# Kernel tuning notes

Hardware: AMD Instinct MI355X
Metric: run time of the kernel (lower is better)

The kernel has to match this reference:

```python
import math
import jax, jax.numpy as jnp
import numpy as np

N = 1600; C_IN = 16; HID = 64; OUT = 64; D_K = 8; N_HEADS = 8
CUTS = 8; NUM_RBF = 8; RBF_PROJ = 4; RADIUS = 6.0; ALPHA = 3.0

def leaky(x):
    return jnp.where(x >= 0, x, 0.2 * x)

def group_norm(x, gamma, beta, groups=4, eps=1e-5):
    # x: [N, C]; torch GroupNorm applied on [1, C, N]: stats over (C/groups, N) per group
    n, c = x.shape
    xg = x.T.reshape(groups, -1)
    mu = jnp.mean(xg, axis=1, keepdims=True)
    var = jnp.mean((xg - mu) ** 2, axis=1, keepdims=True)
    xn = ((xg - mu) * jax.lax.rsqrt(var + eps)).reshape(c, n).T
    return xn * gamma + beta

def setup_inputs():
    key = jax.random.key(0)
    ks = jax.random.split(key, 32)
    def rn(k, shape, s=0.1):
        return (jax.random.normal(k, shape) * s).astype(jnp.float32)
    return {
        "points": jax.random.normal(ks[0], (N, 3), jnp.float32),
        "nuv": jax.random.normal(ks[1], (N, 3, 3), jnp.float32),
        "features": jax.random.normal(ks[2], (N, C_IN), jnp.float32),
        "w_in1": rn(ks[3], (HID, C_IN)), "b_in1": rn(ks[4], (HID,)),
        "w_in2": rn(ks[5], (HID, HID)), "b_in2": rn(ks[6], (HID,)),
        "g_in": 1.0 + rn(ks[7], (HID,)), "be_in": rn(ks[8], (HID,)),
        "wq": rn(ks[9], (HID, HID)), "bq": rn(ks[10], (HID,)),
        "wk": rn(ks[11], (HID, HID)), "bk": rn(ks[12], (HID,)),
        "wv": rn(ks[13], (HID, HID)), "bv": rn(ks[14], (HID,)),
        "conv_w1": rn(ks[15], (CUTS, 4 + RBF_PROJ), 0.5),
        "conv_b1": jnp.abs(rn(ks[16], (CUTS,), 0.5)),
        "conv_w2": rn(ks[17], (HID, CUTS), 0.3), "conv_b2": rn(ks[18], (HID,), 0.3),
        "rbf_log_sigma": jnp.log(jnp.asarray(0.6 * 2.0 / (NUM_RBF - 1), jnp.float32)),
        "rbf_a": rn(ks[19], (RBF_PROJ, NUM_RBF), 0.3), "rbf_b": rn(ks[20], (RBF_PROJ,), 0.1),
        "rbf_centers": jnp.linspace(0.0, 2.0, NUM_RBF, dtype=jnp.float32),
        "w_o1": rn(ks[21], (OUT, HID)), "b_o1": rn(ks[22], (OUT,)),
        "w_o2": rn(ks[23], (OUT, OUT)), "b_o2": rn(ks[24], (OUT,)),
        "g_out": 1.0 + rn(ks[25], (OUT,)), "be_out": rn(ks[26], (OUT,)),
        "w_res": rn(ks[27], (OUT, C_IN)), "b_res": rn(ks[28], (OUT,)),
    }

def reference(points, nuv, features, w_in1, b_in1, w_in2, b_in2, g_in, be_in,
              wq, bq, wk, bk, wv, bv, conv_w1, conv_b1, conv_w2, conv_b2,
              rbf_log_sigma, rbf_a, rbf_b, rbf_centers,
              w_o1, b_o1, w_o2, b_o2, g_out, be_out, w_res, b_res):
    # point-wise MLP + GroupNorm
    h = leaky(features @ w_in1.T + b_in1)
    h = leaky(h @ w_in2.T + b_in2)
    h = group_norm(h, g_in, be_in)
    Q = h @ wq.T + bq
    K = h @ wk.T + bk
    V = h @ wv.T + bv
    pts = points / (math.sqrt(2.0) * RADIUS)
    diff = pts[None, :, :] - pts[:, None, :]            # [N, N, 3] = x_j - x_i
    n_i = nuv[:, 0, :]
    n_j = jax.lax.stop_gradient(n_i)                    # j-side normals are detached in the original
    ndot = jnp.einsum("ia,ja->ij", n_i, n_j)            # <n_i, n_j>
    d2 = jnp.sum(diff ** 2, axis=-1) * (2.0 - ndot) ** 2  # pseudo-geodesic squared distance
    W = (1.0 + d2 / ALPHA) ** (-ALPHA)                  # geodesic window weight
    d2_safe = jnp.where(d2 > 0, d2, 1.0)
    base_d = jnp.where(d2 > 0, jnp.sqrt(d2_safe), 0.0)  # safe sqrt (finite grad at 0)
    sigma = jnp.maximum(jnp.exp(rbf_log_sigma), 1e-6)
    R = jnp.exp(-((base_d[:, :, None] - rbf_centers) ** 2) / (2.0 * sigma ** 2))  # [N,N,NUM_RBF]
    R_proj = R @ rbf_a.T + rbf_b                        # [N, N, RBF_PROJ]
    X_loc = jnp.einsum("iab,ijb->ija", nuv, diff)       # local tangent-frame coords [N,N,3]
    X = jnp.concatenate([X_loc, ndot[:, :, None], R_proj], axis=-1)  # [N, N, 4+RBF_PROJ]
    F1 = jax.nn.relu(X @ conv_w1.T + conv_b1)           # shared conv layer-1 [N, N, CUTS]
    scale = 1.0 / math.sqrt(D_K)
    heads = []
    for h_id in range(N_HEADS):
        s = slice(h_id * D_K, (h_id + 1) * D_K)
        Fh = jax.nn.relu(F1 @ conv_w2[s].T + conv_b2[s])      # per-head conv weights [N, N, D_K]
        S = (Q[:, s] @ K[:, s].T) * scale                     # attention logits [N, N]
        P = jax.nn.softmax(S, axis=1) * W                     # softmax over j, fused with window
        heads.append(jnp.einsum("ij,ijc,jc->ic", P, Fh, V[:, s]))
    agg = jnp.concatenate(heads, axis=1)                      # [N, HID]
    o = leaky(agg @ w_o1.T + b_o1)
    o = leaky(o @ w_o2.T + b_o2)
    o = group_norm(o, g_out, be_out)
    return o + features @ w_res.T + b_res
```

## Files before the change

### kernel.cpp

```cpp
#include <hip/hip_runtime.h>

typedef __fp16 h2 __attribute__((ext_vector_type(2)));
typedef unsigned int u32;
typedef unsigned short u16;

#define NPTS 1600
#define NCHUNK 10
#define CHUNKJ 160
#define TILE 32
#define QS (0.35355339059327373f*1.4426950408889634f)
#define PSCALE 0.11785113019775793f
#define LOG2E 1.4426950408889634f

__device__ __forceinline__ float leaky(float x){ return x >= 0.f ? x : 0.2f*x; }
__device__ __forceinline__ float d4(float4 a, float4 b){ return a.x*b.x + a.y*b.y + a.z*b.z + a.w*b.w; }
__device__ __forceinline__ u32 pkn(float a, float b){ h2 v; v[0]=(__fp16)a; v[1]=(__fp16)b; return __builtin_bit_cast(u32,v); }
__device__ __forceinline__ h2 u2h(u32 u){ return __builtin_bit_cast(h2,u); }
__device__ __forceinline__ float dot2(h2 a, h2 b, float c){ return __builtin_amdgcn_fdot2(a,b,c,false); }
__device__ __forceinline__ u32 rfl(u32 x){ return (u32)__builtin_amdgcn_readfirstlane((int)x); }

__global__ __launch_bounds__(256) void k_in(
    const float* __restrict__ feat, const float* __restrict__ w1, const float* __restrict__ b1,
    const float* __restrict__ w2, const float* __restrict__ b2,
    const float* __restrict__ conv_w1, const float* __restrict__ conv_b1,
    const float* __restrict__ conv_w2,
    const float* __restrict__ rbf_a, const float* __restrict__ rbf_b,
    const float* __restrict__ rbf_ls, const float* __restrict__ rbf_c,
    float* __restrict__ h2out, float* __restrict__ bstat1, float* __restrict__ wpk)
{
  __shared__ float sh[4][64];
  __shared__ float sred[4][8];
  int t = threadIdx.x, w = t>>6, c = t&63;
  int i = blockIdx.x*4 + w;

  if (blockIdx.x == 0) {
    u32* wp = (u32*)wpk;
    {
      int row = t>>2, q = t&3;
      wp[32 + row*4 + q] = pkn(conv_w2[row*8+2*q], conv_w2[row*8+2*q+1]);
    }
    if (t < 32) {
      int cc = t>>2, kq = t&3;
      float a0=0.f, a1=0.f;
      #pragma unroll
      for (int p=0;p<4;p++){ a0 += conv_w1[cc*8+4+p]*rbf_a[p*8+2*kq]; a1 += conv_w1[cc*8+4+p]*rbf_a[p*8+2*kq+1]; }
      wp[cc*4+kq] = pkn(a0,a1);
    } else if (t < 40) {
      int cc = t-32; float s = conv_b1[cc];
      #pragma unroll
      for (int p=0;p<4;p++) s += conv_w1[cc*8+4+p]*rbf_b[p];
      wpk[288+cc] = s;
    } else if (t == 40) {
      float sig = fmaxf(expf(rbf_ls[0]), 1e-6f);
      float m = -LOG2E/(2.f*sig*sig);
      float c0 = rbf_c[0];
      float dl = rbf_c[1] - rbf_c[0];
      float A1v = m*dl*dl;
      wpk[296] = c0;
      wpk[297] = m;
      wpk[298] = -2.f*m*dl;
      wpk[299] = A1v;
      float Av = exp2f(A1v);
      wpk[300] = Av;
      wpk[301] = Av*Av;
    }
  }

  const float4* f4 = (const float4*)(feat + i*16);
  float4 f0=f4[0], f1v=f4[1], f2v=f4[2], f3v=f4[3];
  const float4* w1r = (const float4*)(w1 + c*16);
  float h1 = b1[c] + d4(f0,w1r[0]) + d4(f1v,w1r[1]) + d4(f2v,w1r[2]) + d4(f3v,w1r[3]);
  h1 = leaky(h1);
  sh[w][c] = h1;
  __syncthreads();
  float hh = b2[c];
  #pragma unroll
  for (int k4=0;k4<16;k4++){
    float4 hv = *(const float4*)&sh[w][k4*4];
    hh += d4(hv, *(const float4*)&w2[c*64 + k4*4]);
  }
  hh = leaky(hh);
  h2out[i*64+c] = hh;

  float s = hh, qq = hh*hh;
  s += __shfl_xor(s,1);  qq += __shfl_xor(qq,1);
  s += __shfl_xor(s,2);  qq += __shfl_xor(qq,2);
  s += __shfl_xor(s,4);  qq += __shfl_xor(qq,4);
  s += __shfl_xor(s,8);  qq += __shfl_xor(qq,8);
  if ((c&15)==0){ int g=c>>4; sred[w][g]=s; sred[w][4+g]=qq; }
  __syncthreads();
  if (t<8) bstat1[blockIdx.x*8+t] = sred[0][t]+sred[1][t]+sred[2][t]+sred[3][t];
}

__global__ __launch_bounds__(256) void k_qkv(
  const float* __restrict__ h2b, const float* __restrict__ bstat1,
  const float* __restrict__ g_in, const float* __restrict__ be_in,
  const float* __restrict__ wq, const float* __restrict__ bq,
  const float* __restrict__ wk, const float* __restrict__ bk,
  const float* __restrict__ wv, const float* __restrict__ bv,
  const float* __restrict__ pts, const float* __restrict__ nuv,
  u32* __restrict__ Q16, u32* __restrict__ K16, u32* __restrict__ V16,
  float* __restrict__ PN)
{
  __shared__ float sh[4][64];
  __shared__ float sp[64];
  __shared__ float sst[8];
  int t=threadIdx.x, w=t>>6, c=t&63;
  int i = blockIdx.x*4 + w;
  if (t<64){ int g=t&7; float s=0.f;
    for (int m=t>>3; m<400; m+=8) s += bstat1[m*8+g];
    sp[t]=s; }
  __syncthreads();
  if (t<8){ float s=0.f;
    #pragma unroll
    for (int q=0;q<8;q++) s += sp[q*8+t];
    sst[t]=s; }
  __syncthreads();
  int g = c>>4;
  const float inv = 1.f/25600.f;
  float mu = sst[g]*inv;
  float var = sst[4+g]*inv - mu*mu;
  float rs = rsqrtf(var + 1e-5f);
  float hn = (h2b[i*64+c]-mu)*rs*g_in[c] + be_in[c];
  sh[w][c] = hn;
  __syncthreads();
  float q=bq[c], k=bk[c], v=bv[c];
  #pragma unroll
  for (int k4=0;k4<16;k4++){
    float4 hv = *(const float4*)&sh[w][k4*4];
    q += d4(hv, *(const float4*)&wq[c*64+k4*4]);
    k += d4(hv, *(const float4*)&wk[c*64+k4*4]);
    v += d4(hv, *(const float4*)&wv[c*64+k4*4]);
  }
  u16* Q16u = (u16*)Q16;
  u16* K16u = (u16*)K16;
  u16* V16u = (u16*)V16;
  __fp16 qh = (__fp16)(q*QS);
  __fp16 kh = (__fp16)k;
  __fp16 vh = (__fp16)v;
  Q16u[i*64 + c] = __builtin_bit_cast(u16, qh);
  K16u[i*64 + c] = __builtin_bit_cast(u16, kh);
  int pr = ((i>>5)<<4) + (i&15);
  int hf = (i>>4)&1;
  V16u[(pr*64 + c)*2 + hf] = __builtin_bit_cast(u16, vh);
  if (c < 6){
    float pv = (c<3) ? pts[i*3+c]*PSCALE : nuv[i*9+(c-3)];
    PN[i*8+c] = pv;
  } else if (c < 8) PN[i*8+c] = 0.f;
}

__global__ __launch_bounds__(256) void k_pair(
  const u32* __restrict__ Q16, const u32* __restrict__ K16, const u32* __restrict__ V16,
  const float* __restrict__ PN, const float* __restrict__ nuv,
  const float* __restrict__ w1, const float* __restrict__ wpk,
  const float* __restrict__ b2g, float* __restrict__ part)
{
  __shared__ __align__(16) u32   sQ16[16*36];
  __shared__ __align__(16) u32   sWX[16*20];
  __shared__ __align__(16) float sRedH[4*16*36];

  int t = threadIdx.x;
  int r = t & 15, jl = t >> 4;
  int bx = blockIdx.x;
  int rb = bx % 100, jc = bx / 100;
  int I0 = rb*16, J0 = jc*CHUNKJ;
  int i = I0 + r;

  if (t < 128) {
    int qrow = t>>3, qq4 = (t&7)<<2;
    *(uint4*)&sQ16[qrow*36+qq4] = *(const uint4*)&Q16[(I0+qrow)*32+qq4];
  }
  if (t < 128) {
    int r2 = t>>3, cc = t&7, ib = (I0+r2)*9;
    float a0=w1[cc*8], a1=w1[cc*8+1], a2=w1[cc*8+2];
    float x = a0*nuv[ib+0] + a1*nuv[ib+3] + a2*nuv[ib+6];
    float y = a0*nuv[ib+1] + a1*nuv[ib+4] + a2*nuv[ib+7];
    float z = a0*nuv[ib+2] + a1*nuv[ib+5] + a2*nuv[ib+8];
    sWX[r2*20+cc*2+0] = pkn(x,y);
    sWX[r2*20+cc*2+1] = pkn(z, w1[cc*8+3]);
  }
  __syncthreads();

  const u32* wp = (const u32*)wpk;
  h2 wr[8][4];
  #pragma unroll
  for (int cc=0;cc<8;cc++)
    #pragma unroll
    for (int q2=0;q2<4;q2++) wr[cc][q2] = u2h(rfl(wp[cc*4+q2]));
  const u32* w2p = wp + 32;
  const float* b1p = wpk + 288;
  float c0  = wpk[296];
  float mco = wpk[297];
  float C2  = wpk[298];
  float Af  = wpk[300];
  float A2f = wpk[301];

  float4 pni0 = *(const float4*)&PN[i*8];
  float4 pni1 = *(const float4*)&PN[i*8+4];
  float pix = pni0.x, piy = pni0.y, piz = pni0.z;
  float nix = pni0.w, niy = pni1.x, niz = pni1.y;

  #pragma unroll 1
  for (int hp=0; hp<2; hp++) {
    float acc[32];
    #pragma unroll
    for (int o=0;o<32;o++) acc[o] = 0.f;
    float lh[4] = {0.f,0.f,0.f,0.f};

    #pragma unroll 1
    for (int tb=0; tb<CHUNKJ; tb+=TILE) {
      int jbase = J0 + tb;
      int jA = jbase + jl;
      int jB = jA + 16;

      h2 F1p[2][4];
      float Wv[2];
      #pragma unroll
      for (int jj=0;jj<2;jj++) {
        int j = jj ? jB : jA;
        float4 a0 = *(const float4*)&PN[j*8];
        float4 a1 = *(const float4*)&PN[j*8+4];
        float dx = a0.x-pix, dy = a0.y-piy, dz = a0.z-piz;
        float ndot = nix*a0.w + niy*a1.x + niz*a1.y;
        float d2r = dx*dx + dy*dy + dz*dz;
        float wf = 2.f - ndot;
        float d2 = d2r*wf*wf;
        float tp = fmaf(d2, 0.3333333333333333f, 1.f);
        Wv[jj] = __builtin_amdgcn_rcpf(tp*tp*tp);
        float dd = __builtin_amdgcn_sqrtf(d2);
        float g0 = dd - c0;
        float E = __builtin_amdgcn_exp2f(mco*g0*g0);
        float U = __builtin_amdgcn_exp2f(C2*g0);
        float R[8];
        R[0] = E;
        float tt = U*Af;
        #pragma unroll
        for (int k=1;k<8;k++){ R[k] = R[k-1]*tt; tt *= A2f; }
        h2 xv0; xv0[0]=(__fp16)dx; xv0[1]=(__fp16)dy;
        h2 xv1; xv1[0]=(__fp16)dz; xv1[1]=(__fp16)ndot;
        h2 r01=__builtin_amdgcn_cvt_pkrtz(R[0],R[1]);
        h2 r23=__builtin_amdgcn_cvt_pkrtz(R[2],R[3]);
        h2 r45=__builtin_amdgcn_cvt_pkrtz(R[4],R[5]);
        h2 r67=__builtin_amdgcn_cvt_pkrtz(R[6],R[7]);
        float F1f[8];
        #pragma unroll
        for (int cc=0;cc<8;cc++){
          uint2 wx2 = *(const uint2*)&sWX[r*20+cc*2];
          float fa = dot2(r01, wr[cc][0], dot2(r23, wr[cc][1], b1p[cc]));
          float fb = dot2(r45, wr[cc][2], dot2(r67, wr[cc][3], 0.f));
          float fc = dot2(u2h(wx2.x), xv0, dot2(u2h(wx2.y), xv1, 0.f));
          F1f[cc] = fmaxf(fa+fb+fc, 0.f);
        }
        F1p[jj][0]=__builtin_amdgcn_cvt_pkrtz(F1f[0],F1f[1]);
        F1p[jj][1]=__builtin_amdgcn_cvt_pkrtz(F1f[2],F1f[3]);
        F1p[jj][2]=__builtin_amdgcn_cvt_pkrtz(F1f[4],F1f[5]);
        F1p[jj][3]=__builtin_amdgcn_cvt_pkrtz(F1f[6],F1f[7]);
      }
      h2 Wvp = __builtin_amdgcn_cvt_pkrtz(Wv[0], Wv[1]);

      const u32* kArow = &K16[jA*32];
      const u32* kBrow = &K16[jB*32];
      const u32* vrow  = &V16[(((u32)jbase>>1)+jl)*64];

      #pragma unroll
      for (int hh=0; hh<4; hh++) {
        int h = (hp<<2) + hh;
        uint4 qh = *(const uint4*)&sQ16[r*36 + (h<<2)];
        uint4 kA = *(const uint4*)&kArow[h<<2];
        uint4 kB = *(const uint4*)&kBrow[h<<2];
        float S0 = dot2(u2h(qh.x),u2h(kA.x), dot2(u2h(qh.y),u2h(kA.y), 0.f))
                 + dot2(u2h(qh.z),u2h(kA.z), dot2(u2h(qh.w),u2h(kA.w), 0.f));
        float S1 = dot2(u2h(qh.x),u2h(kB.x), dot2(u2h(qh.y),u2h(kB.y), 0.f))
                 + dot2(u2h(qh.z),u2h(kB.z), dot2(u2h(qh.w),u2h(kB.w), 0.f));
        float e0 = __builtin_amdgcn_exp2f(S0);
        float e1 = __builtin_amdgcn_exp2f(S1);
        lh[hh] += e0 + e1;
        h2 ewp = __builtin_amdgcn_cvt_pkrtz(e0,e1) * Wvp;
        uint4 vpA = *(const uint4*)&vrow[h*8];
        uint4 vpB = *(const uint4*)&vrow[h*8+4];
        u32 vparr[8] = {vpA.x,vpA.y,vpA.z,vpA.w,vpB.x,vpB.y,vpB.z,vpB.w};
        #pragma unroll
        for (int cc=0;cc<8;cc++){
          int rw = h*8+cc;
          h2 w0=u2h(w2p[rw*4+0]), w1h=u2h(w2p[rw*4+1]), w2h=u2h(w2p[rw*4+2]), w3h=u2h(w2p[rw*4+3]);
          float b2v = b2g[rw];
          float fh0 = dot2(F1p[0][0],w0, dot2(F1p[0][1],w1h, b2v))
                    + dot2(F1p[0][2],w2h, dot2(F1p[0][3],w3h, 0.f));
          float fh1 = dot2(F1p[1][0],w0, dot2(F1p[1][1],w1h, b2v))
                    + dot2(F1p[1][2],w2h, dot2(F1p[1][3],w3h, 0.f));
          h2 fhp = __builtin_amdgcn_cvt_pkrtz(fmaxf(fh0,0.f), fmaxf(fh1,0.f));
          h2 ev = u2h(vparr[cc]) * ewp;
          acc[hh*8+cc] = dot2(fhp, ev, acc[hh*8+cc]);
        }
      }
    }

    #pragma unroll
    for (int o=0;o<32;o++){ acc[o] += __shfl_xor(acc[o],16); acc[o] += __shfl_xor(acc[o],32); }
    #pragma unroll
    for (int hh=0;hh<4;hh++){ lh[hh] += __shfl_xor(lh[hh],16); lh[hh] += __shfl_xor(lh[hh],32); }
    __syncthreads();
    int wv = t >> 6, lane = t & 63;
    if (lane < 16) {
      #pragma unroll
      for (int o=0;o<32;o++) sRedH[(wv*16+lane)*36+o] = acc[o];
      #pragma unroll
      for (int hh=0;hh<4;hh++) sRedH[(wv*16+lane)*36+32+hh] = lh[hh];
    }
    __syncthreads();
    for (int v2 = t; v2 < 16*36; v2 += 256) {
      int rr = v2/36, o = v2 - rr*36;
      float s = sRedH[(0*16+rr)*36+o]+sRedH[(1*16+rr)*36+o]+sRedH[(2*16+rr)*36+o]+sRedH[(3*16+rr)*36+o];
      int off = (o < 32) ? (hp<<5)+o : 64 + (hp<<2) + (o-32);
      part[(jc*NPTS + I0 + rr)*72 + off] = s;
    }
  }
}

__global__ __launch_bounds__(256) void k_agg(
  const float* __restrict__ part, const float* __restrict__ w_o1, const float* __restrict__ b_o1,
  const float* __restrict__ w_o2, const float* __restrict__ b_o2,
  float* __restrict__ o2b, float* __restrict__ bstat2)
{
  __shared__ float sh[4][64];
  __shared__ float sred[4][8];
  int t = threadIdx.x, w = t>>6, c = t&63;
  int i = blockIdx.x*4 + w;
  int h = c>>3;
  float a = 0.f, L = 0.f;
  #pragma unroll
  for (int jc=0;jc<NCHUNK;jc++){
    const float* p = part + (jc*NPTS + i)*72;
    a += p[c]; L += p[64+h];
  }
  float agg = a / L;
  sh[w][c] = agg; __syncthreads();
  float o1 = b_o1[c];
  #pragma unroll
  for (int k4=0;k4<16;k4++){
    float4 hv = *(const float4*)&sh[w][k4*4];
    o1 += d4(hv, *(const float4*)&w_o1[c*64+k4*4]);
  }
  o1 = leaky(o1);
  __syncthreads();
  sh[w][c] = o1; __syncthreads();
  float o2 = b_o2[c];
  #pragma unroll
  for (int k4=0;k4<16;k4++){
    float4 hv = *(const float4*)&sh[w][k4*4];
    o2 += d4(hv, *(const float4*)&w_o2[c*64+k4*4]);
  }
  o2 = leaky(o2);
  o2b[i*64+c] = o2;

  float s = o2, qq = o2*o2;
  s += __shfl_xor(s,1);  qq += __shfl_xor(qq,1);
  s += __shfl_xor(s,2);  qq += __shfl_xor(qq,2);
  s += __shfl_xor(s,4);  qq += __shfl_xor(qq,4);
  s += __shfl_xor(s,8);  qq += __shfl_xor(qq,8);
  if ((c&15)==0){ int g=c>>4; sred[w][g]=s; sred[w][4+g]=qq; }
  __syncthreads();
  if (t<8) bstat2[blockIdx.x*8+t] = sred[0][t]+sred[1][t]+sred[2][t]+sred[3][t];
}

__global__ __launch_bounds__(256) void k_out(
  const float* __restrict__ o2b, const float* __restrict__ bstat2,
  const float* __restrict__ g_out, const float* __restrict__ be_out,
  const float* __restrict__ feat, const float* __restrict__ w_res, const float* __restrict__ b_res,
  float* __restrict__ out)
{
  __shared__ float sp[64];
  __shared__ float sst[8];
  int t = threadIdx.x, w = t>>6, c = t&63;
  int i = blockIdx.x*4 + w;
  if (t<64){ int g=t&7; float s=0.f;
    for (int m=t>>3; m<400; m+=8) s += bstat2[m*8+g];
    sp[t]=s; }
  __syncthreads();
  if (t<8){ float s=0.f;
    #pragma unroll
    for (int q=0;q<8;q++) s += sp[q*8+t];
    sst[t]=s; }
  __syncthreads();
  int g = c>>4;
  const float inv = 1.f/25600.f;
  float mu = sst[g]*inv;
  float var = sst[4+g]*inv - mu*mu;
  float rs = rsqrtf(var + 1e-5f);
  float on = (o2b[i*64+c]-mu)*rs*g_out[c] + be_out[c];
  const float4* f4 = (const float4*)(feat + i*16);
  const float4* wr = (const float4*)(w_res + c*16);
  float res = b_res[c] + d4(f4[0],wr[0]) + d4(f4[1],wr[1]) + d4(f4[2],wr[2]) + d4(f4[3],wr[3]);
  out[i*64+c] = on + res;
}

extern "C" void kernel_launch(void* const* d_in, const int* in_sizes, int n_in,
                              void* d_out, int out_size, void* d_ws, size_t ws_size,
                              hipStream_t stream) {
  const float* points  = (const float*)d_in[0];
  const float* nuv     = (const float*)d_in[1];
  const float* feat    = (const float*)d_in[2];
  const float* w_in1   = (const float*)d_in[3];
  const float* b_in1   = (const float*)d_in[4];
  const float* w_in2   = (const float*)d_in[5];
  const float* b_in2   = (const float*)d_in[6];
  const float* g_in    = (const float*)d_in[7];
  const float* be_in   = (const float*)d_in[8];
  const float* wq      = (const float*)d_in[9];
  const float* bq      = (const float*)d_in[10];
  const float* wk      = (const float*)d_in[11];
  const float* bk      = (const float*)d_in[12];
  const float* wv      = (const float*)d_in[13];
  const float* bv      = (const float*)d_in[14];
  const float* conv_w1 = (const float*)d_in[15];
  const float* conv_b1 = (const float*)d_in[16];
  const float* conv_w2 = (const float*)d_in[17];
  const float* conv_b2 = (const float*)d_in[18];
  const float* rbf_ls  = (const float*)d_in[19];
  const float* rbf_a   = (const float*)d_in[20];
  const float* rbf_b   = (const float*)d_in[21];
  const float* rbf_c   = (const float*)d_in[22];
  const float* w_o1    = (const float*)d_in[23];
  const float* b_o1    = (const float*)d_in[24];
  const float* w_o2    = (const float*)d_in[25];
  const float* b_o2    = (const float*)d_in[26];
  const float* g_out   = (const float*)d_in[27];
  const float* be_out  = (const float*)d_in[28];
  const float* w_res   = (const float*)d_in[29];
  const float* b_res   = (const float*)d_in[30];

  float* ws     = (float*)d_ws;
  float* h2f    = ws;
  u32*   Q16    = (u32*)(ws + 102400);
  u32*   K16    = (u32*)(ws + 153600);
  u32*   V16    = (u32*)(ws + 204800);
  float* PN     = ws + 256000;
  float* bstat1 = ws + 268800;
  float* bstat2 = ws + 272000;
  float* wpk    = ws + 275200;
  float* part   = ws + 275520;
  float* o2b    = ws + 1427520;
  float* out    = (float*)d_out;

  k_in<<<400, 256, 0, stream>>>(feat, w_in1, b_in1, w_in2, b_in2,
                                conv_w1, conv_b1, conv_w2, rbf_a, rbf_b, rbf_ls, rbf_c,
                                h2f, bstat1, wpk);
  k_qkv<<<400, 256, 0, stream>>>(h2f, bstat1, g_in, be_in, wq, bq, wk, bk, wv, bv,
                                 points, nuv, Q16, K16, V16, PN);
  k_pair<<<1000, 256, 0, stream>>>(Q16, K16, V16, PN, nuv, conv_w1, wpk, conv_b2, part);
  k_agg<<<400, 256, 0, stream>>>(part, w_o1, b_o1, w_o2, b_o2, o2b, bstat2);
  k_out<<<400, 256, 0, stream>>>(o2b, bstat2, g_out, be_out, feat, w_res, b_res, out);
}
```

Baseline: 262.9 us.

## Fuse head-pair passes in pair kernel and widen blocks to 512 threads

The pair kernel used to make two passes over the j-chunk, four heads per pass, and so recomputed the geometric features (distances, RBF, conv layer 1) twice. It now keeps all 8 heads' 64 accumulators in registers and makes a single pass. Blocks grow to 512 threads with 320-wide j chunks, so half as many partial results are written and summed in k_agg, and the V layout is reshaped to match the 64-wide tile. The cost is a much larger register footprint per thread, which may lower occupancy or cause spills, and fewer blocks in the grid.

```diff
diff --git a/kernel.cpp b/kernel.cpp
--- a/kernel.cpp
+++ b/kernel.cpp
@@ -5,9 +5,9 @@
 typedef unsigned short u16;
 
 #define NPTS 1600
-#define NCHUNK 10
-#define CHUNKJ 160
-#define TILE 32
+#define NCHUNK 5
+#define CHUNKJ 320
+#define TILE 64
 #define QS (0.35355339059327373f*1.4426950408889634f)
 #define PSCALE 0.11785113019775793f
 #define LOG2E 1.4426950408889634f
@@ -140,8 +140,8 @@
   __fp16 vh = (__fp16)v;
   Q16u[i*64 + c] = __builtin_bit_cast(u16, qh);
   K16u[i*64 + c] = __builtin_bit_cast(u16, kh);
-  int pr = ((i>>5)<<4) + (i&15);
-  int hf = (i>>4)&1;
+  int pr = ((i>>6)<<5) + (i&31);
+  int hf = (i>>5)&1;
   V16u[(pr*64 + c)*2 + hf] = __builtin_bit_cast(u16, vh);
   if (c < 6){
     float pv = (c<3) ? pts[i*3+c]*PSCALE : nuv[i*9+(c-3)];
@@ -149,15 +149,16 @@
   } else if (c < 8) PN[i*8+c] = 0.f;
 }
 
-__global__ __launch_bounds__(256) void k_pair(
+__global__ __launch_bounds__(512) void k_pair(
   const u32* __restrict__ Q16, const u32* __restrict__ K16, const u32* __restrict__ V16,
   const float* __restrict__ PN, const float* __restrict__ nuv,
   const float* __restrict__ w1, const float* __restrict__ wpk,
   const float* __restrict__ b2g, float* __restrict__ part)
 {
-  __shared__ __align__(16) u32   sQ16[16*36];
-  __shared__ __align__(16) u32   sWX[16*20];
-  __shared__ __align__(16) float sRedH[4*16*36];
+  __shared__ __align__(16) float SM[8*16*72];
+  u32* sQ16 = (u32*)SM;
+  u32* sWX  = (u32*)SM + 576;
+  float* sRed = SM;
 
   int t = threadIdx.x;
   int r = t & 15, jl = t >> 4;
@@ -200,120 +201,119 @@
   float pix = pni0.x, piy = pni0.y, piz = pni0.z;
   float nix = pni0.w, niy = pni1.x, niz = pni1.y;
 
+  float acc[64];
+  #pragma unroll
+  for (int o=0;o<64;o++) acc[o] = 0.f;
+  float lh[8];
+  #pragma unroll
+  for (int h=0;h<8;h++) lh[h] = 0.f;
+
   #pragma unroll 1
-  for (int hp=0; hp<2; hp++) {
-    float acc[32];
-    #pragma unroll
-    for (int o=0;o<32;o++) acc[o] = 0.f;
-    float lh[4] = {0.f,0.f,0.f,0.f};
-
-    #pragma unroll 1
-    for (int tb=0; tb<CHUNKJ; tb+=TILE) {
-      int jbase = J0 + tb;
-      int jA = jbase + jl;
-      int jB = jA + 16;
-
-      h2 F1p[2][4];
-      float Wv[2];
+  for (int tb=0; tb<CHUNKJ; tb+=TILE) {
+    int jbase = J0 + tb;
+    int jA = jbase + jl;
+    int jB = jA + 32;
+
+    h2 F1p[2][4];
+    float Wv[2];
+    #pragma unroll
+    for (int jj=0;jj<2;jj++) {
+      int j = jj ? jB : jA;
+      float4 a0 = *(const float4*)&PN[j*8];
+      float4 a1 = *(const float4*)&PN[j*8+4];
+      float dx = a0.x-pix, dy = a0.y-piy, dz = a0.z-piz;
+      float ndot = nix*a0.w + niy*a1.x + niz*a1.y;
+      float d2r = dx*dx + dy*dy + dz*dz;
+      float wf = 2.f - ndot;
+      float d2 = d2r*wf*wf;
+      float tp = fmaf(d2, 0.3333333333333333f, 1.f);
+      Wv[jj] = __builtin_amdgcn_rcpf(tp*tp*tp);
+      float dd = __builtin_amdgcn_sqrtf(d2);
+      float g0 = dd - c0;
+      float E = __builtin_amdgcn_exp2f(mco*g0*g0);
+      float U = __builtin_amdgcn_exp2f(C2*g0);
+      float R[8];
+      R[0] = E;
+      float tt = U*Af;
       #pragma unroll
-      for (int jj=0;jj<2;jj++) {
-        int j = jj ? jB : jA;
-        float4 a0 = *(const float4*)&PN[j*8];
-        float4 a1 = *(const float4*)&PN[j*8+4];
-        float dx = a0.x-pix, dy = a0.y-piy, dz = a0.z-piz;
-        float ndot = nix*a0.w + niy*a1.x + niz*a1.y;
-        float d2r = dx*dx + dy*dy + dz*dz;
-        float wf = 2.f - ndot;
-        float d2 = d2r*wf*wf;
-        float tp = fmaf(d2, 0.3333333333333333f, 1.f);
-        Wv[jj] = __builtin_amdgcn_rcpf(tp*tp*tp);
-        float dd = __builtin_amdgcn_sqrtf(d2);
-        float g0 = dd - c0;
-        float E = __builtin_amdgcn_exp2f(mco*g0*g0);
-        float U = __builtin_amdgcn_exp2f(C2*g0);
-        float R[8];
-        R[0] = E;
-        float tt = U*Af;
-        #pragma unroll
-        for (int k=1;k<8;k++){ R[k] = R[k-1]*tt; tt *= A2f; }
-        h2 xv0; xv0[0]=(__fp16)dx; xv0[1]=(__fp16)dy;
-        h2 xv1; xv1[0]=(__fp16)dz; xv1[1]=(__fp16)ndot;
-        h2 r01=__builtin_amdgcn_cvt_pkrtz(R[0],R[1]);
-        h2 r23=__builtin_amdgcn_cvt_pkrtz(R[2],R[3]);
-        h2 r45=__builtin_amdgcn_cvt_pkrtz(R[4],R[5]);
-        h2 r67=__builtin_amdgcn_cvt_pkrtz(R[6],R[7]);
-        float F1f[8];
-        #pragma unroll
-        for (int cc=0;cc<8;cc++){
-          uint2 wx2 = *(const uint2*)&sWX[r*20+cc*2];
-          float fa = dot2(r01, wr[cc][0], dot2(r23, wr[cc][1], b1p[cc]));
-          float fb = dot2(r45, wr[cc][2], dot2(r67, wr[cc][3], 0.f));
-          float fc = dot2(u2h(wx2.x), xv0, dot2(u2h(wx2.y), xv1, 0.f));
-          F1f[cc] = fmaxf(fa+fb+fc, 0.f);
-        }
-        F1p[jj][0]=__builtin_amdgcn_cvt_pkrtz(F1f[0],F1f[1]);
-        F1p[jj][1]=__builtin_amdgcn_cvt_pkrtz(F1f[2],F1f[3]);
-        F1p[jj][2]=__builtin_amdgcn_cvt_pkrtz(F1f[4],F1f[5]);
-        F1p[jj][3]=__builtin_amdgcn_cvt_pkrtz(F1f[6],F1f[7]);
+      for (int k=1;k<8;k++){ R[k] = R[k-1]*tt; tt *= A2f; }
+      h2 xv0; xv0[0]=(__fp16)dx; xv0[1]=(__fp16)dy;
+      h2 xv1; xv1[0]=(__fp16)dz; xv1[1]=(__fp16)ndot;
+      h2 r01=__builtin_amdgcn_cvt_pkrtz(R[0],R[1]);
+      h2 r23=__builtin_amdgcn_cvt_pkrtz(R[2],R[3]);
+      h2 r45=__builtin_amdgcn_cvt_pkrtz(R[4],R[5]);
+      h2 r67=__builtin_amdgcn_cvt_pkrtz(R[6],R[7]);
+      float F1f[8];
+      #pragma unroll
+      for (int cc=0;cc<8;cc++){
+        uint2 wx2 = *(const uint2*)&sWX[r*20+cc*2];
+        float fa = dot2(r01, wr[cc][0], dot2(r23, wr[cc][1], b1p[cc]));
+        float fb = dot2(r45, wr[cc][2], dot2(r67, wr[cc][3], 0.f));
+        float fc = dot2(u2h(wx2.x), xv0, dot2(u2h(wx2.y), xv1, 0.f));
+        F1f[cc] = fmaxf(fa+fb+fc, 0.f);
       }
-      h2 Wvp = __builtin_amdgcn_cvt_pkrtz(Wv[0], Wv[1]);
-
-      const u32* kArow = &K16[jA*32];
-      const u32* kBrow = &K16[jB*32];
-      const u32* vrow  = &V16[(((u32)jbase>>1)+jl)*64];
-
+      F1p[jj][0]=__builtin_amdgcn_cvt_pkrtz(F1f[0],F1f[1]);
+      F1p[jj][1]=__builtin_amdgcn_cvt_pkrtz(F1f[2],F1f[3]);
+      F1p[jj][2]=__builtin_amdgcn_cvt_pkrtz(F1f[4],F1f[5]);
+      F1p[jj][3]=__builtin_amdgcn_cvt_pkrtz(F1f[6],F1f[7]);
+    }
+    h2 Wvp = __builtin_amdgcn_cvt_pkrtz(Wv[0], Wv[1]);
+
+    const u32* kArow = &K16[jA*32];
+    const u32* kBrow = &K16[jB*32];
+    const u32* vrow  = &V16[(((u32)jbase>>1)+jl)*64];
+
+    #pragma unroll
+    for (int h=0;h<8;h++) {
+      uint4 qh = *(const uint4*)&sQ16[r*36 + (h<<2)];
+      uint4 kA = *(const uint4*)&kArow[h<<2];
+      uint4 kB = *(const uint4*)&kBrow[h<<2];
+      float S0 = dot2(u2h(qh.x),u2h(kA.x), dot2(u2h(qh.y),u2h(kA.y), 0.f))
+               + dot2(u2h(qh.z),u2h(kA.z), dot2(u2h(qh.w),u2h(kA.w), 0.f));
+      float S1 = dot2(u2h(qh.x),u2h(kB.x), dot2(u2h(qh.y),u2h(kB.y), 0.f))
+               + dot2(u2h(qh.z),u2h(kB.z), dot2(u2h(qh.w),u2h(kB.w), 0.f));
+      float e0 = __builtin_amdgcn_exp2f(S0);
+      float e1 = __builtin_amdgcn_exp2f(S1);
+      lh[h] += e0 + e1;
+      h2 ewp = __builtin_amdgcn_cvt_pkrtz(e0,e1) * Wvp;
+      uint4 vpA = *(const uint4*)&vrow[h*8];
+      uint4 vpB = *(const uint4*)&vrow[h*8+4];
+      u32 vparr[8] = {vpA.x,vpA.y,vpA.z,vpA.w,vpB.x,vpB.y,vpB.z,vpB.w};
       #pragma unroll
-      for (int hh=0; hh<4; hh++) {
-        int h = (hp<<2) + hh;
-        uint4 qh = *(const uint4*)&sQ16[r*36 + (h<<2)];
-        uint4 kA = *(const uint4*)&kArow[h<<2];
-        uint4 kB = *(const uint4*)&kBrow[h<<2];
-        float S0 = dot2(u2h(qh.x),u2h(kA.x), dot2(u2h(qh.y),u2h(kA.y), 0.f))
-                 + dot2(u2h(qh.z),u2h(kA.z), dot2(u2h(qh.w),u2h(kA.w), 0.f));
-        float S1 = dot2(u2h(qh.x),u2h(kB.x), dot2(u2h(qh.y),u2h(kB.y), 0.f))
-                 + dot2(u2h(qh.z),u2h(kB.z), dot2(u2h(qh.w),u2h(kB.w), 0.f));
-        float e0 = __builtin_amdgcn_exp2f(S0);
-        float e1 = __builtin_amdgcn_exp2f(S1);
-        lh[hh] += e0 + e1;
-        h2 ewp = __builtin_amdgcn_cvt_pkrtz(e0,e1) * Wvp;
-        uint4 vpA = *(const uint4*)&vrow[h*8];
-        uint4 vpB = *(const uint4*)&vrow[h*8+4];
-        u32 vparr[8] = {vpA.x,vpA.y,vpA.z,vpA.w,vpB.x,vpB.y,vpB.z,vpB.w};
-        #pragma unroll
-        for (int cc=0;cc<8;cc++){
-          int rw = h*8+cc;
-          h2 w0=u2h(w2p[rw*4+0]), w1h=u2h(w2p[rw*4+1]), w2h=u2h(w2p[rw*4+2]), w3h=u2h(w2p[rw*4+3]);
-          float b2v = b2g[rw];
-          float fh0 = dot2(F1p[0][0],w0, dot2(F1p[0][1],w1h, b2v))
-                    + dot2(F1p[0][2],w2h, dot2(F1p[0][3],w3h, 0.f));
-          float fh1 = dot2(F1p[1][0],w0, dot2(F1p[1][1],w1h, b2v))
-                    + dot2(F1p[1][2],w2h, dot2(F1p[1][3],w3h, 0.f));
-          h2 fhp = __builtin_amdgcn_cvt_pkrtz(fmaxf(fh0,0.f), fmaxf(fh1,0.f));
-          h2 ev = u2h(vparr[cc]) * ewp;
-          acc[hh*8+cc] = dot2(fhp, ev, acc[hh*8+cc]);
-        }
+      for (int cc=0;cc<8;cc++){
+        int rw = h*8+cc;
+        h2 w0=u2h(w2p[rw*4+0]), w1h=u2h(w2p[rw*4+1]), w2h=u2h(w2p[rw*4+2]), w3h=u2h(w2p[rw*4+3]);
+        float b2v = b2g[rw];
+        float fh0 = dot2(F1p[0][0],w0, dot2(F1p[0][1],w1h, b2v))
+                  + dot2(F1p[0][2],w2h, dot2(F1p[0][3],w3h, 0.f));
+        float fh1 = dot2(F1p[1][0],w0, dot2(F1p[1][1],w1h, b2v))
+                  + dot2(F1p[1][2],w2h, dot2(F1p[1][3],w3h, 0.f));
+        h2 fhp = __builtin_amdgcn_cvt_pkrtz(fmaxf(fh0,0.f), fmaxf(fh1,0.f));
+        h2 ev = u2h(vparr[cc]) * ewp;
+        acc[rw] = dot2(fhp, ev, acc[rw]);
       }
     }
-
-    #pragma unroll
-    for (int o=0;o<32;o++){ acc[o] += __shfl_xor(acc[o],16); acc[o] += __shfl_xor(acc[o],32); }
-    #pragma unroll
-    for (int hh=0;hh<4;hh++){ lh[hh] += __shfl_xor(lh[hh],16); lh[hh] += __shfl_xor(lh[hh],32); }
-    __syncthreads();
-    int wv = t >> 6, lane = t & 63;
-    if (lane < 16) {
-      #pragma unroll
-      for (int o=0;o<32;o++) sRedH[(wv*16+lane)*36+o] = acc[o];
-      #pragma unroll
-      for (int hh=0;hh<4;hh++) sRedH[(wv*16+lane)*36+32+hh] = lh[hh];
-    }
-    __syncthreads();
-    for (int v2 = t; v2 < 16*36; v2 += 256) {
-      int rr = v2/36, o = v2 - rr*36;
-      float s = sRedH[(0*16+rr)*36+o]+sRedH[(1*16+rr)*36+o]+sRedH[(2*16+rr)*36+o]+sRedH[(3*16+rr)*36+o];
-      int off = (o < 32) ? (hp<<5)+o : 64 + (hp<<2) + (o-32);
-      part[(jc*NPTS + I0 + rr)*72 + off] = s;
-    }
+  }
+
+  #pragma unroll
+  for (int o=0;o<64;o++){ acc[o] += __shfl_xor(acc[o],16); acc[o] += __shfl_xor(acc[o],32); }
+  #pragma unroll
+  for (int h=0;h<8;h++){ lh[h] += __shfl_xor(lh[h],16); lh[h] += __shfl_xor(lh[h],32); }
+  __syncthreads();
+  int wv = t >> 6, lane = t & 63;
+  if (lane < 16) {
+    #pragma unroll
+    for (int o=0;o<64;o++) sRed[(wv*16+lane)*72+o] = acc[o];
+    #pragma unroll
+    for (int h=0;h<8;h++) sRed[(wv*16+lane)*72+64+h] = lh[h];
+  }
+  __syncthreads();
+  for (int v2 = t; v2 < 16*72; v2 += 512) {
+    int rr = v2/72, o = v2 - rr*72;
+    float s = 0.f;
+    #pragma unroll
+    for (int q=0;q<8;q++) s += sRed[(q*16+rr)*72+o];
+    part[(jc*NPTS + I0 + rr)*72 + o] = s;
   }
 }
 
@@ -439,7 +439,7 @@
   float* bstat2 = ws + 272000;
   float* wpk    = ws + 275200;
   float* part   = ws + 275520;
-  float* o2b    = ws + 1427520;
+  float* o2b    = ws + 851520;
   float* out    = (float*)d_out;
 
   k_in<<<400, 256, 0, stream>>>(feat, w_in1, b_in1, w_in2, b_in2,
@@ -447,7 +447,7 @@
                                 h2f, bstat1, wpk);
   k_qkv<<<400, 256, 0, stream>>>(h2f, bstat1, g_in, be_in, wq, bq, wk, bk, wv, bv,
                                  points, nuv, Q16, K16, V16, PN);
-  k_pair<<<1000, 256, 0, stream>>>(Q16, K16, V16, PN, nuv, conv_w1, wpk, conv_b2, part);
+  k_pair<<<500, 512, 0, stream>>>(Q16, K16, V16, PN, nuv, conv_w1, wpk, conv_b2, part);
   k_agg<<<400, 256, 0, stream>>>(part, w_o1, b_o1, w_o2, b_o2, o2b, bstat2);
   k_out<<<400, 256, 0, stream>>>(o2b, bstat2, g_out, be_out, feat, w_res, b_res, out);
 }
```

After: 258.3 us. No clear change (-1.7%).
